# Performance work log

Hardware: AMD Instinct MI355X
Metric: run time of the kernel (lower is better)

The kernel has to match this reference:

```python
import jax, jax.numpy as jnp
import numpy as np

EPS = 1e-5
NUM_HEADS = 20


def ln(x, w, b=None):
    m = x.mean(-1, keepdims=True)
    v = x.var(-1, keepdims=True)
    y = (x - m) * jax.lax.rsqrt(v + EPS) * w
    return y + b if b is not None else y


def rotate_half(t):
    t1, t2 = jnp.split(t, 2, axis=-1)
    return jnp.concatenate([-t2, t1], axis=-1)


def setup_inputs() -> dict:
    key = jax.random.key(0)
    B, S, E = 8, 1024, 1280  # 8 packed sequences of length 1024, ESM-2 650M width
    T = B * S
    ks = jax.random.split(key, 6)
    scale = (1.0 / E) ** 0.5  # ~xavier scale
    w = lambda k: jax.random.normal(k, (E, E), jnp.float32) * scale
    return {
        "x": jax.random.normal(ks[0], (T, E), jnp.float32),
        "cu_lens": jnp.arange(B + 1, dtype=jnp.int32) * S,
        "max_len": S,
        "norm_w": jnp.ones((E,), jnp.float32),
        "norm_b": jnp.zeros((E,), jnp.float32),
        "Wq": w(ks[1]),
        "Wk": w(ks[2]),
        "Wv": w(ks[3]),
        "Wout": w(ks[4]),
        "lnq_w": jnp.ones((E,), jnp.float32),
        "lnk_w": jnp.ones((E,), jnp.float32),
    }


def reference(x, cu_lens, max_len, norm_w, norm_b, Wq, Wk, Wv, Wout, lnq_w, lnk_w):
    T, E = x.shape
    H = NUM_HEADS
    D = E // H

    # pre-norm + separate Q/K/V projections (bias=False)
    h = ln(x, norm_w, norm_b)
    q = ln(h @ Wq.T, lnq_w)   # per-head-stack LayerNorm on q (no bias)
    k = ln(h @ Wk.T, lnk_w)
    v = h @ Wv.T

    q = q.reshape(T, H, D)
    k = k.reshape(T, H, D)
    v = v.reshape(T, H, D)

    # rotary embedding: positions restart at each sequence boundary (cu_lens)
    tok = jnp.arange(T)
    seg = jnp.searchsorted(cu_lens, tok, side="right") - 1
    pos = (tok - cu_lens[seg]).astype(jnp.float32)
    inv_freq = 1.0 / (10000.0 ** (jnp.arange(0, D, 2, dtype=jnp.float32) / D))
    f = pos[:, None] * inv_freq[None, :]                      # [T, D/2]
    cos = jnp.concatenate([jnp.cos(f), jnp.cos(f)], -1)[:, None, :]  # [T,1,D]
    sin = jnp.concatenate([jnp.sin(f), jnp.sin(f)], -1)[:, None, :]
    q = q * cos + rotate_half(q) * sin
    k = k * cos + rotate_half(k) * sin

    # varlen flash attention; sequences are equal-length here so reshape to
    # [B,S,...] which exactly honors the block-diagonal (no cross-sequence) mask
    B = cu_lens.shape[0] - 1
    S = T // B
    qb = q.reshape(B, S, H, D)
    kb = k.reshape(B, S, H, D)
    vb = v.reshape(B, S, H, D)

    scores = jnp.einsum("bqhd,bkhd->bhqk", qb, kb) * (D ** -0.5)
    attn = jax.nn.softmax(scores, axis=-1)
    o = jnp.einsum("bhqk,bkhd->bqhd", attn, vb).reshape(T, E)
    return o @ Wout.T
```

## Files before the change

### kernel.cpp

```cpp
#include <hip/hip_runtime.h>
#include <hip/hip_bf16.h>
#include <math.h>

#define NH 20
#define HD 64
#define E_DIM 1280
#define T_TOK 8192
#define NSEQ 8
#define N4 (E_DIM * E_DIM / 4)

#define SCALE_LOG2 0.1803368801111204f

typedef unsigned short u16;
typedef unsigned int u32;
typedef __attribute__((ext_vector_type(8))) short bf16x8;
typedef __attribute__((ext_vector_type(4))) float f32x4;
typedef __attribute__((ext_vector_type(16))) float f32x16;

__device__ __forceinline__ float bf2f(u16 h) {
  union { float f; unsigned u; } c; c.u = ((unsigned)h) << 16; return c.f;
}
__device__ __forceinline__ u16 f2bf(float f) {
  union { float f; unsigned u; } c; c.f = f;
  unsigned u = c.u;
  return (u16)((u + 0x7fffu + ((u >> 16) & 1u)) >> 16);
}
__device__ __forceinline__ u32 cvtpk(float lo, float hi) {
  u32 r;
  asm("v_cvt_pk_bf16_f32 %0, %1, %2" : "=v"(r) : "v"(lo), "v"(hi));
  return r;
}

__device__ __forceinline__ void gld_lds16(const void* g, void* l) {
  __builtin_amdgcn_global_load_lds((const __attribute__((address_space(1))) void*)g,
                                   (__attribute__((address_space(3))) void*)l,
                                   16, 0, 0);
}

#define BARR() __builtin_amdgcn_s_barrier()
#define LGKM0() do { asm volatile("s_waitcnt lgkmcnt(0)" ::: "memory"); \
                     __builtin_amdgcn_sched_barrier(0); } while (0)
#define VMC4() asm volatile("s_waitcnt vmcnt(4)" ::: "memory")
#define VMC0() asm volatile("s_waitcnt vmcnt(0)" ::: "memory")

__global__ __launch_bounds__(256) void cvt_all(const float* __restrict__ Wq,
                                               const float* __restrict__ Wk,
                                               const float* __restrict__ Wv,
                                               const float* __restrict__ Wo,
                                               u16* __restrict__ wqkv,
                                               u16* __restrict__ wo) {
  int i = blockIdx.x * 256 + threadIdx.x;
  if (i >= 4 * N4) return;
  int r = i / N4;
  int l = i - r * N4;
  const float* src = (r == 0) ? Wq : (r == 1) ? Wk : (r == 2) ? Wv : Wo;
  float4 v = ((const float4*)src)[l];
  ushort4 ov;
  ov.x = f2bf(v.x); ov.y = f2bf(v.y); ov.z = f2bf(v.z); ov.w = f2bf(v.w);
  if (r < 3) ((ushort4*)wqkv)[(size_t)r * N4 + l] = ov;
  else       ((ushort4*)wo)[l] = ov;
}

__global__ __launch_bounds__(256) void rope_tab_kernel(float2* __restrict__ tab) {
  int i = blockIdx.x * 256 + threadIdx.x;
  if (i >= 1024 * 32) return;
  int pos = i >> 5, dm = i & 31;
  float freq = exp2f(-(float)dm * (13.287712379549449f / 32.0f));
  float f = (float)pos * freq;
  tab[i] = make_float2(cosf(f), sinf(f));
}

__global__ __launch_bounds__(320) void ln_x_kernel(const float* __restrict__ x,
                                                   const float* __restrict__ w,
                                                   const float* __restrict__ b,
                                                   u16* __restrict__ h) {
  const int row = blockIdx.x;
  const int tid = threadIdx.x;
  const float4 xv = ((const float4*)(x + (size_t)row * E_DIM))[tid];
  float s  = xv.x + xv.y + xv.z + xv.w;
  float s2 = xv.x*xv.x + xv.y*xv.y + xv.z*xv.z + xv.w*xv.w;
#pragma unroll
  for (int m = 1; m < 64; m <<= 1) { s += __shfl_xor(s, m); s2 += __shfl_xor(s2, m); }
  __shared__ float ss[5], ss2[5];
  if ((tid & 63) == 0) { ss[tid >> 6] = s; ss2[tid >> 6] = s2; }
  __syncthreads();
  s  = ss[0] + ss[1] + ss[2] + ss[3] + ss[4];
  s2 = ss2[0] + ss2[1] + ss2[2] + ss2[3] + ss2[4];
  const float mean = s * (1.0f / E_DIM);
  const float var  = s2 * (1.0f / E_DIM) - mean * mean;
  const float rstd = rsqrtf(var + 1e-5f);
  const float4 wv = ((const float4*)w)[tid];
  const float4 bv = ((const float4*)b)[tid];
  ushort4 o;
  o.x = f2bf((xv.x - mean) * rstd * wv.x + bv.x);
  o.y = f2bf((xv.y - mean) * rstd * wv.y + bv.y);
  o.z = f2bf((xv.z - mean) * rstd * wv.z + bv.z);
  o.w = f2bf((xv.w - mean) * rstd * wv.w + bv.w);
  ((ushort4*)(h + (size_t)row * E_DIM))[tid] = o;
}

__global__ __launch_bounds__(320) void ln_rope_kernel(const u16* __restrict__ pre,
                                                      const float* __restrict__ w,
                                                      const int* __restrict__ cu,
                                                      const float2* __restrict__ tab,
                                                      u16* __restrict__ outq,
                                                      float oscale) {
  const int row = blockIdx.x;
  const int tid = threadIdx.x;
  __shared__ float y[E_DIM];
  const ushort4 qv = ((const ushort4*)(pre + (size_t)row * E_DIM))[tid];
  float v0 = bf2f(qv.x), v1 = bf2f(qv.y), v2 = bf2f(qv.z), v3 = bf2f(qv.w);
  float s  = v0 + v1 + v2 + v3;
  float s2 = v0*v0 + v1*v1 + v2*v2 + v3*v3;
#pragma unroll
  for (int m = 1; m < 64; m <<= 1) { s += __shfl_xor(s, m); s2 += __shfl_xor(s2, m); }
  __shared__ float ss[5], ss2[5];
  if ((tid & 63) == 0) { ss[tid >> 6] = s; ss2[tid >> 6] = s2; }
  __syncthreads();
  s  = ss[0] + ss[1] + ss[2] + ss[3] + ss[4];
  s2 = ss2[0] + ss2[1] + ss2[2] + ss2[3] + ss2[4];
  const float mean = s * (1.0f / E_DIM);
  const float var  = s2 * (1.0f / E_DIM) - mean * mean;
  const float rstd = rsqrtf(var + 1e-5f) ;
  const int e0 = tid * 4;
  float4 wv = ((const float4*)w)[tid];
  wv.x *= oscale; wv.y *= oscale; wv.z *= oscale; wv.w *= oscale;
  y[e0 + 0] = (v0 - mean) * rstd * wv.x;
  y[e0 + 1] = (v1 - mean) * rstd * wv.y;
  y[e0 + 2] = (v2 - mean) * rstd * wv.z;
  y[e0 + 3] = (v3 - mean) * rstd * wv.w;
  __syncthreads();
  int seg = 0;
#pragma unroll
  for (int bb = 1; bb < NSEQ + 1; bb++) if (cu[bb] <= row) seg = bb;
  const int pos = row - cu[seg];
  const int d0 = e0 & 63;
  const int hbase = e0 - d0;
  const float4* tp = (const float4*)(tab + pos * 32 + (d0 & 31));
  const float4 t0 = tp[0], t1 = tp[1];
  const float cs_[4] = {t0.x, t0.z, t1.x, t1.z};
  const float sn_[4] = {t0.y, t0.w, t1.y, t1.w};
  const bool lo = (d0 < 32);
  ushort4 o;
#pragma unroll
  for (int i = 0; i < 4; i++) {
    const int d = d0 + i;
    float r;
    if (lo) r = y[hbase + d] * cs_[i] - y[hbase + d + 32] * sn_[i];
    else    r = y[hbase + d] * cs_[i] + y[hbase + d - 32] * sn_[i];
    ((u16*)&o)[i] = f2bf(r);
  }
  ((ushort4*)(outq + (size_t)row * E_DIM))[tid] = o;
}

template <int MODE, int K>
__global__ __launch_bounds__(512) void gemm256(const u16* __restrict__ A,
                                               const u16* __restrict__ B,
                                               u16* __restrict__ preq,
                                               u16* __restrict__ prek,
                                               u16* __restrict__ vT,
                                               float* __restrict__ Cf) {
  __shared__ u16 As[2][16384];
  __shared__ u16 Bs[2][16384];
  const int tid = threadIdx.x;
  const int wid = tid >> 6, lane = tid & 63;
  const int l16 = lane & 15, lq = lane >> 4;
  const int wm = wid >> 2, wn = wid & 3;
  const int bm = blockIdx.x & 31;
  const int bn = blockIdx.x >> 5;
  const int m0 = bm << 8, n0 = bn << 8;
  const int sw = l16 & 7;

  const int row0 = tid >> 3;
  const int ch0 = ((tid & 7) ^ (row0 & 7)) << 3;
  const u16* Abase = A + (size_t)(m0 + row0) * K + ch0;
  const u16* Bbase = B + (size_t)(n0 + row0) * K + ch0;
  const int dst0 = tid * 8;

  const int CA = (wm * 128 + l16) * 64;
  const int CB = (wn * 64 + l16) * 64;
  const int ch_0 = ((0 | lq) ^ sw) << 3;
  const int ch_1 = ((4 | lq) ^ sw) << 3;

  f32x4 acc[8][4] = {};
  bf16x8 aF[4][2], bF[2][2][2];

#define STG(Larr, bufp, hh, gbase, kt) do {                                     \
    const u16* g_ = (gbase) + (size_t)(hh) * 128 * K + (size_t)(kt) * 64;       \
    gld_lds16(g_, &Larr[bufp][(hh) * 8192 + dst0]);                             \
    gld_lds16(g_ + (size_t)64 * K, &Larr[bufp][(hh) * 8192 + dst0 + 4096]);     \
  } while (0)

#define RDA(bufp, a) do {                                                       \
    _Pragma("unroll") for (int mb = 0; mb < 4; mb++) {                          \
      aF[mb][0] = *(const bf16x8*)(&As[bufp][CA + (a) * 4096 + mb * 1024 + ch_0]); \
      aF[mb][1] = *(const bf16x8*)(&As[bufp][CA + (a) * 4096 + mb * 1024 + ch_1]); \
    } } while (0)

#define RDB(bufp, b) do {                                                       \
    _Pragma("unroll") for (int nb = 0; nb < 2; nb++) {                          \
      bF[b][nb][0] = *(const bf16x8*)(&Bs[bufp][CB + (b) * 2048 + nb * 1024 + ch_0]); \
      bF[b][nb][1] = *(const bf16x8*)(&Bs[bufp][CB + (b) * 2048 + nb * 1024 + ch_1]); \
    } } while (0)

#define MFQ(a, b) do {                                                          \
    __builtin_amdgcn_s_setprio(1);                                              \
    _Pragma("unroll") for (int mb = 0; mb < 4; mb++)                            \
    _Pragma("unroll") for (int nb = 0; nb < 2; nb++)                            \
    _Pragma("unroll") for (int kk = 0; kk < 2; kk++)                            \
      acc[(a) * 4 + mb][(b) * 2 + nb] = __builtin_amdgcn_mfma_f32_16x16x32_bf16( \
          aF[mb][kk], bF[b][nb][kk], acc[(a) * 4 + mb][(b) * 2 + nb], 0, 0, 0); \
    __builtin_amdgcn_s_setprio(0); } while (0)

  STG(Bs, 0, 0, Bbase, 0);
  STG(As, 0, 0, Abase, 0);
  STG(Bs, 0, 1, Bbase, 0);
  STG(As, 0, 1, Abase, 0);
  STG(Bs, 1, 0, Bbase, 1);
  STG(As, 1, 0, Abase, 1);
  VMC4();
  BARR();

  const int NIT = K / 128;
  for (int i = 0; i < NIT; i++) {
    const bool lastI = (i == NIT - 1);
    const int k1 = 2 * i + 1, k2 = 2 * i + 2, k3 = 2 * i + 3;
    RDA(0, 0); RDB(0, 0);
    STG(Bs, 1, 1, Bbase, k1);
    BARR(); LGKM0(); MFQ(0, 0); BARR();
    RDB(0, 1);
    STG(As, 1, 1, Abase, k1);
    BARR(); LGKM0(); MFQ(0, 1); BARR();
    RDA(0, 1);
    if (!lastI) STG(Bs, 0, 0, Bbase, k2);
    BARR(); LGKM0(); MFQ(1, 0); BARR();
    if (!lastI) { STG(As, 0, 0, Abase, k2); VMC4(); } else { VMC0(); }
    BARR(); LGKM0(); MFQ(1, 1); BARR();
    RDA(1, 0); RDB(1, 0);
    if (!lastI) STG(Bs, 0, 1, Bbase, k2);
    BARR(); LGKM0(); MFQ(0, 0); BARR();
    RDB(1, 1);
    if (!lastI) STG(As, 0, 1, Abase, k2);
    BARR(); LGKM0(); MFQ(0, 1); BARR();
    RDA(1, 1);
    if (!lastI) STG(Bs, 1, 0, Bbase, k3);
    BARR(); LGKM0(); MFQ(1, 0); BARR();
    if (!lastI) {
      STG(As, 1, 0, Abase, k3);
      VMC4();
      BARR(); LGKM0(); MFQ(1, 1); BARR();
    } else {
      LGKM0(); MFQ(1, 1);
    }
  }
#undef STG
#undef RDA
#undef RDB
#undef MFQ

  if (MODE == 0) {
    if (n0 < 2560) {
      u16* dst; int c0;
      if (n0 < 1280) { dst = preq; c0 = n0; }
      else           { dst = prek; c0 = n0 - 1280; }
#pragma unroll
      for (int mi = 0; mi < 8; mi++)
#pragma unroll
        for (int j = 0; j < 4; j++) {
          const size_t rowo = (size_t)(m0 + wm * 128 + mi * 16 + lq * 4 + j) * E_DIM;
#pragma unroll
          for (int ni = 0; ni < 4; ni++)
            dst[rowo + c0 + wn * 64 + ni * 16 + l16] = f2bf(acc[mi][ni][j]);
        }
    } else {
      const int c0 = n0 - 2560;
#pragma unroll
      for (int mi = 0; mi < 8; mi++)
#pragma unroll
        for (int ni = 0; ni < 4; ni++) {
          ushort4 pkt;
          pkt.x = f2bf(acc[mi][ni][0]); pkt.y = f2bf(acc[mi][ni][1]);
          pkt.z = f2bf(acc[mi][ni][2]); pkt.w = f2bf(acc[mi][ni][3]);
          const size_t off = (size_t)(c0 + wn * 64 + ni * 16 + l16) * T_TOK +
                             (m0 + wm * 128 + mi * 16 + lq * 4);
          *(ushort4*)(vT + off) = pkt;
        }
    }
  } else {
#pragma unroll
    for (int mi = 0; mi < 8; mi++)
#pragma unroll
      for (int j = 0; j < 4; j++) {
        const size_t rowo = (size_t)(m0 + wm * 128 + mi * 16 + lq * 4 + j) * E_DIM;
#pragma unroll
        for (int ni = 0; ni < 4; ni++)
          Cf[rowo + n0 + wn * 64 + ni * 16 + l16] = acc[mi][ni][j];
      }
  }
}

__global__ __launch_bounds__(256) void attn_kernel(const u16* __restrict__ q,
                                                   const u16* __restrict__ k,
                                                   const u16* __restrict__ vT,
                                                   const int* __restrict__ cu,
                                                   u16* __restrict__ o) {
  const int bx = blockIdx.x;
  const int hb = bx % (NH * NSEQ);
  const int qt = bx / (NH * NSEQ);
  const int hh = hb % NH;
  const int b  = hb / NH;
  const int base = cu[b];
  const int nkt  = (cu[b + 1] - base) >> 6;
  const int tid  = threadIdx.x;
  const int wid  = tid >> 6, lane = tid & 63;
  const int l31  = lane & 31, hi = lane >> 5;

  __shared__ u16 Ks[2][64 * 64];
  __shared__ u16 Vs[2][64 * 64];

  const int qrow = base + qt * 128 + wid * 32 + l31;
  bf16x8 qf[4];
#pragma unroll
  for (int kk = 0; kk < 4; kk++)
    qf[kk] = *(const bf16x8*)(q + (size_t)qrow * E_DIM + hh * 64 + kk * 16 + hi * 8);

  f32x16 acc0 = {}, acc1 = {};
  float lrow = 0.f;

  const int r0 = tid >> 3;
  const int chs = tid & 7;
  const int cs0 = (chs ^ (r0 & 7)) << 3;
  const int r1 = r0 + 32;
  const int cs1 = (chs ^ (r1 & 7)) << 3;
  const u16* kg0 = k  + (size_t)(base + r0) * E_DIM + hh * 64 + cs0;
  const u16* kg1 = k  + (size_t)(base + r1) * E_DIM + hh * 64 + cs1;
  const u16* vg0 = vT + (size_t)(hh * 64 + r0) * T_TOK + base + cs0;
  const u16* vg1 = vT + (size_t)(hh * 64 + r1) * T_TOK + base + cs1;
  const int ldsoff = wid * 512;

  gld_lds16(kg0, &Ks[0][ldsoff]);
  gld_lds16(kg1, &Ks[0][2048 + ldsoff]);
  gld_lds16(vg0, &Vs[0][ldsoff]);
  gld_lds16(vg1, &Vs[0][2048 + ldsoff]);
  __syncthreads();

  int cur = 0;
  for (int kt = 0; kt < nkt; kt++) {
    if (kt + 1 < nkt) {
      const size_t ko = (size_t)(kt + 1) * 64 * E_DIM;
      const int vo = (kt + 1) * 64;
      u16* kd = Ks[cur ^ 1];
      u16* vd = Vs[cur ^ 1];
      gld_lds16(kg0 + ko, kd + ldsoff);
      gld_lds16(kg1 + ko, kd + 2048 + ldsoff);
      gld_lds16(vg0 + vo, vd + ldsoff);
      gld_lds16(vg1 + vo, vd + 2048 + ldsoff);
    }
    const u16* Kc = Ks[cur];
    const u16* Vc = Vs[cur];

    f32x16 S0 = {}, S1 = {};
#pragma unroll
    for (int kk = 0; kk < 4; kk++) {
      const int c0 = (((kk << 1) | hi) ^ (l31 & 7)) << 3;
      const bf16x8 kf0 = *(const bf16x8*)(Kc + l31 * 64 + c0);
      const bf16x8 kf1 = *(const bf16x8*)(Kc + (32 + l31) * 64 + c0);
      S0 = __builtin_amdgcn_mfma_f32_32x32x16_bf16(kf0, qf[kk], S0, 0, 0, 0);
      S1 = __builtin_amdgcn_mfma_f32_32x32x16_bf16(kf1, qf[kk], S1, 0, 0, 0);
    }

    float rs0 = 0.f, rs1 = 0.f, rs2 = 0.f, rs3 = 0.f;
#pragma unroll
    for (int r = 0; r < 16; r += 4) {
      S0[r + 0] = exp2f(S0[r + 0]); S0[r + 1] = exp2f(S0[r + 1]);
      S0[r + 2] = exp2f(S0[r + 2]); S0[r + 3] = exp2f(S0[r + 3]);
      rs0 += S0[r + 0]; rs1 += S0[r + 1]; rs2 += S0[r + 2]; rs3 += S0[r + 3];
    }
#pragma unroll
    for (int r = 0; r < 16; r += 4) {
      S1[r + 0] = exp2f(S1[r + 0]); S1[r + 1] = exp2f(S1[r + 1]);
      S1[r + 2] = exp2f(S1[r + 2]); S1[r + 3] = exp2f(S1[r + 3]);
      rs0 += S1[r + 0]; rs1 += S1[r + 1]; rs2 += S1[r + 2]; rs3 += S1[r + 3];
    }
    float rs = (rs0 + rs1) + (rs2 + rs3);
    rs += __shfl_xor(rs, 32);
    lrow += rs;

    u32 pw[4][4];
#pragma unroll
    for (int ks = 0; ks < 4; ks++) {
      const int g = (ks & 1) << 3;
      u32 A0, A1, B0, B1;
      if (ks < 2) {
        A0 = cvtpk(S0[g + 0], S0[g + 1]); A1 = cvtpk(S0[g + 2], S0[g + 3]);
        B0 = cvtpk(S0[g + 4], S0[g + 5]); B1 = cvtpk(S0[g + 6], S0[g + 7]);
      } else {
        A0 = cvtpk(S1[g + 0], S1[g + 1]); A1 = cvtpk(S1[g + 2], S1[g + 3]);
        B0 = cvtpk(S1[g + 4], S1[g + 5]); B1 = cvtpk(S1[g + 6], S1[g + 7]);
      }
      asm("v_permlane32_swap_b32 %0, %1" : "+v"(A0), "+v"(B0));
      asm("v_permlane32_swap_b32 %0, %1" : "+v"(A1), "+v"(B1));
      pw[ks][0] = A0; pw[ks][1] = A1; pw[ks][2] = B0; pw[ks][3] = B1;
    }

#pragma unroll
    for (int ks = 0; ks < 4; ks++) {
      const bf16x8 pa = *(const bf16x8*)&pw[ks][0];
      const int c0 = (((ks << 1) | hi) ^ (l31 & 7)) << 3;
      const bf16x8 vf0 = *(const bf16x8*)(Vc + l31 * 64 + c0);
      const bf16x8 vf1 = *(const bf16x8*)(Vc + (32 + l31) * 64 + c0);
      acc0 = __builtin_amdgcn_mfma_f32_32x32x16_bf16(pa, vf0, acc0, 0, 0, 0);
      acc1 = __builtin_amdgcn_mfma_f32_32x32x16_bf16(pa, vf1, acc1, 0, 0, 0);
    }
    __syncthreads();
    cur ^= 1;
  }

  const float linv = 1.0f / lrow;
  const int tok0 = base + qt * 128 + wid * 32;
#pragma unroll
  for (int r = 0; r < 16; r++) {
    const int qr = (r & 3) + 8 * (r >> 2) + 4 * hi;
    const float ls = __shfl(linv, qr);
    const size_t ro = (size_t)(tok0 + qr) * E_DIM + hh * 64 + l31;
    o[ro]      = f2bf(acc0[r] * ls);
    o[ro + 32] = f2bf(acc1[r] * ls);
  }
}

extern "C" void kernel_launch(void* const* d_in, const int* in_sizes, int n_in,
                              void* d_out, int out_size, void* d_ws, size_t ws_size,
                              hipStream_t stream) {
  const float* x      = (const float*)d_in[0];
  const int*   cu     = (const int*)d_in[1];
  const float* norm_w = (const float*)d_in[3];
  const float* norm_b = (const float*)d_in[4];
  const float* Wq     = (const float*)d_in[5];
  const float* Wk     = (const float*)d_in[6];
  const float* Wv     = (const float*)d_in[7];
  const float* Wo     = (const float*)d_in[8];
  const float* lnq    = (const float*)d_in[9];
  const float* lnk    = (const float*)d_in[10];
  float* out = (float*)d_out;

  const size_t EE2 = (size_t)E_DIM * E_DIM * 2;
  const size_t TE2 = (size_t)T_TOK * E_DIM * 2;
  char* p = (char*)d_ws;
  u16* wqkv = (u16*)p; p += 3 * EE2;
  u16* wo_b = (u16*)p; p += EE2;
  u16* h_b  = (u16*)p; p += TE2;
  u16* preq = (u16*)p; p += TE2;
  u16* prek = (u16*)p; p += TE2;
  u16* vT_b = (u16*)p; p += TE2;
  float2* tab = (float2*)p; p += 1024 * 32 * sizeof(float2);

  cvt_all<<<(4 * N4 + 255) / 256, 256, 0, stream>>>(Wq, Wk, Wv, Wo, wqkv, wo_b);
  rope_tab_kernel<<<128, 256, 0, stream>>>(tab);
  ln_x_kernel<<<T_TOK, 320, 0, stream>>>(x, norm_w, norm_b, h_b);

  gemm256<0, E_DIM><<<480, 512, 0, stream>>>(h_b, wqkv, preq, prek, vT_b, nullptr);

  ln_rope_kernel<<<T_TOK, 320, 0, stream>>>(preq, lnq, cu, tab, preq, SCALE_LOG2);
  ln_rope_kernel<<<T_TOK, 320, 0, stream>>>(prek, lnk, cu, tab, prek, 1.0f);

  attn_kernel<<<8 * NH * NSEQ, 256, 0, stream>>>(preq, prek, vT_b, cu, h_b);

  gemm256<1, E_DIM><<<160, 512, 0, stream>>>(h_b, wo_b, nullptr, nullptr, nullptr, out);
}
```

Measured before the change: 262.4 us.

## Merge q/k LN-RoPE launches, remap GEMM blocks across XCDs, trim barriers

Merges the two per-row LayerNorm+RoPE launches for q and k into one kernel with twice the grid, selecting the q or k buffer from the block index. Remaps GEMM block IDs so consecutive blocks are spread across the 8 XCDs, each XCD getting a contiguous chunk of tiles to improve L2 reuse. Removes the leading barrier before each MFMA phase and moves the vmcnt wait after the compute, cutting barrier overhead in the GEMM main loop. The barrier removal relies on the remaining barriers still ordering LDS writes and reads correctly across the double buffer.

```diff
diff --git a/kernel.cpp b/kernel.cpp
--- a/kernel.cpp
+++ b/kernel.cpp
@@ -99,13 +99,20 @@
   ((ushort4*)(h + (size_t)row * E_DIM))[tid] = o;
 }
 
-__global__ __launch_bounds__(320) void ln_rope_kernel(const u16* __restrict__ pre,
-                                                      const float* __restrict__ w,
-                                                      const int* __restrict__ cu,
-                                                      const float2* __restrict__ tab,
-                                                      u16* __restrict__ outq,
-                                                      float oscale) {
-  const int row = blockIdx.x;
+__global__ __launch_bounds__(320) void ln_rope2_kernel(const u16* __restrict__ preq,
+                                                       const u16* __restrict__ prek,
+                                                       const float* __restrict__ wq,
+                                                       const float* __restrict__ wk,
+                                                       const int* __restrict__ cu,
+                                                       const float2* __restrict__ tab,
+                                                       u16* __restrict__ outq,
+                                                       u16* __restrict__ outk) {
+  const int sel = blockIdx.x >> 13;
+  const int row = blockIdx.x & (T_TOK - 1);
+  const u16* pre = sel ? prek : preq;
+  const float* w = sel ? wk : wq;
+  u16* outp = sel ? outk : outq;
+  const float oscale = sel ? 1.0f : SCALE_LOG2;
   const int tid = threadIdx.x;
   __shared__ float y[E_DIM];
   const ushort4 qv = ((const ushort4*)(pre + (size_t)row * E_DIM))[tid];
@@ -121,7 +128,7 @@
   s2 = ss2[0] + ss2[1] + ss2[2] + ss2[3] + ss2[4];
   const float mean = s * (1.0f / E_DIM);
   const float var  = s2 * (1.0f / E_DIM) - mean * mean;
-  const float rstd = rsqrtf(var + 1e-5f) ;
+  const float rstd = rsqrtf(var + 1e-5f);
   const int e0 = tid * 4;
   float4 wv = ((const float4*)w)[tid];
   wv.x *= oscale; wv.y *= oscale; wv.z *= oscale; wv.w *= oscale;
@@ -150,7 +157,7 @@
     else    r = y[hbase + d] * cs_[i] + y[hbase + d - 32] * sn_[i];
     ((u16*)&o)[i] = f2bf(r);
   }
-  ((ushort4*)(outq + (size_t)row * E_DIM))[tid] = o;
+  ((ushort4*)(outp + (size_t)row * E_DIM))[tid] = o;
 }
 
 template <int MODE, int K>
@@ -166,8 +173,10 @@
   const int wid = tid >> 6, lane = tid & 63;
   const int l16 = lane & 15, lq = lane >> 4;
   const int wm = wid >> 2, wn = wid & 3;
-  const int bm = blockIdx.x & 31;
-  const int bn = blockIdx.x >> 5;
+  const int cpx = gridDim.x >> 3;
+  const int bid = (blockIdx.x & 7) * cpx + (blockIdx.x >> 3);
+  const int bm = bid & 31;
+  const int bn = bid >> 5;
   const int m0 = bm << 8, n0 = bn << 8;
   const int sw = l16 & 7;
 
@@ -227,28 +236,31 @@
     const int k1 = 2 * i + 1, k2 = 2 * i + 2, k3 = 2 * i + 3;
     RDA(0, 0); RDB(0, 0);
     STG(Bs, 1, 1, Bbase, k1);
-    BARR(); LGKM0(); MFQ(0, 0); BARR();
+    LGKM0(); MFQ(0, 0); BARR();
     RDB(0, 1);
     STG(As, 1, 1, Abase, k1);
-    BARR(); LGKM0(); MFQ(0, 1); BARR();
+    LGKM0(); MFQ(0, 1); BARR();
     RDA(0, 1);
     if (!lastI) STG(Bs, 0, 0, Bbase, k2);
-    BARR(); LGKM0(); MFQ(1, 0); BARR();
-    if (!lastI) { STG(As, 0, 0, Abase, k2); VMC4(); } else { VMC0(); }
-    BARR(); LGKM0(); MFQ(1, 1); BARR();
+    LGKM0(); MFQ(1, 0); BARR();
+    if (!lastI) STG(As, 0, 0, Abase, k2);
+    LGKM0(); MFQ(1, 1);
+    if (!lastI) VMC4(); else VMC0();
+    BARR();
     RDA(1, 0); RDB(1, 0);
     if (!lastI) STG(Bs, 0, 1, Bbase, k2);
-    BARR(); LGKM0(); MFQ(0, 0); BARR();
+    LGKM0(); MFQ(0, 0); BARR();
     RDB(1, 1);
     if (!lastI) STG(As, 0, 1, Abase, k2);
-    BARR(); LGKM0(); MFQ(0, 1); BARR();
+    LGKM0(); MFQ(0, 1); BARR();
     RDA(1, 1);
     if (!lastI) STG(Bs, 1, 0, Bbase, k3);
-    BARR(); LGKM0(); MFQ(1, 0); BARR();
+    LGKM0(); MFQ(1, 0); BARR();
     if (!lastI) {
       STG(As, 1, 0, Abase, k3);
+      LGKM0(); MFQ(1, 1);
       VMC4();
-      BARR(); LGKM0(); MFQ(1, 1); BARR();
+      BARR();
     } else {
       LGKM0(); MFQ(1, 1);
     }
@@ -460,8 +472,7 @@
 
   gemm256<0, E_DIM><<<480, 512, 0, stream>>>(h_b, wqkv, preq, prek, vT_b, nullptr);
 
-  ln_rope_kernel<<<T_TOK, 320, 0, stream>>>(preq, lnq, cu, tab, preq, SCALE_LOG2);
-  ln_rope_kernel<<<T_TOK, 320, 0, stream>>>(prek, lnk, cu, tab, prek, 1.0f);
+  ln_rope2_kernel<<<2 * T_TOK, 320, 0, stream>>>(preq, prek, lnq, lnk, cu, tab, preq, prek);
 
   attn_kernel<<<8 * NH * NSEQ, 256, 0, stream>>>(preq, prek, vT_b, cu, h_b);
 
```

After: 265.0 us. No clear change (+1.0%).
